# Performance work log

Measured on AMD Instinct MI355X. Metric: run time of the kernel, lower is better.

## Reference

```python
import jax, jax.numpy as jnp
import numpy as np


def setup_inputs() -> dict:
    key = jax.random.key(0)
    k1, k2, k3, k4, k5 = jax.random.split(key, 5)
    S, B, He, Hd, A = 2048, 32, 1024, 1024, 512
    dec_out = jax.random.normal(k1, (B, Hd), dtype=jnp.float32)
    enc_outs = jax.random.normal(k2, (S, B, He), dtype=jnp.float32)
    # parameter scales matching nn.Linear default init (~U(-1/sqrt(fan_in), ...))
    W_enc = jax.random.normal(k3, (A, He), dtype=jnp.float32) / np.sqrt(He)
    W_dec = jax.random.normal(k4, (A, Hd), dtype=jnp.float32) / np.sqrt(Hd)
    att_v = jax.random.normal(k5, (A,), dtype=jnp.float32) / np.sqrt(A)
    return {"dec_out": dec_out, "enc_outs": enc_outs, "W_enc": W_enc,
            "W_dec": W_dec, "att_v": att_v}


def reference(dec_out, enc_outs, W_enc, W_dec, att_v):
    # enc_att: (S, B, A) = enc_outs @ W_enc^T
    enc_att = jnp.einsum('sbh,ah->sba', enc_outs, W_enc)
    # dec_att: (B, A) = dec_out @ W_dec^T, tiled over seq_len
    dec_att = jnp.einsum('bh,ah->ba', dec_out, W_dec)
    # additive score: tanh(enc_att + dec_att) . att_v  -> (B, S)
    dec_enc_att = jnp.tanh(enc_att + dec_att[None, :, :])      # (S, B, A)
    scores = jnp.einsum('sba,a->bs', dec_enc_att, att_v)       # (B, S)
    weights = jax.nn.softmax(scores, axis=-1)                  # (B, S)
    # context: weighted sum of encoder outputs -> (B, He)
    context = jnp.einsum('bs,sbh->bh', weights, enc_outs)
    return context, weights
```

## Files before the change

### kernel.cpp

```cpp
#include <hip/hip_runtime.h>
#include <hip/hip_bf16.h>


typedef float f32x4 __attribute__((ext_vector_type(4)));
typedef __bf16 bf16x8 __attribute__((ext_vector_type(8)));

#define WS_DEC_OFF    0u
#define WS_WIMG_OFF   65536u
#define WS_SCORES_OFF (65536u + 1048576u)
#define WS_PART_OFF   (65536u + 1048576u + 262144u)

#define WAITVM10()  asm volatile("s_waitcnt vmcnt(10)" ::: "memory")
#define WAITVM0()   asm volatile("s_waitcnt vmcnt(0)" ::: "memory")
#define WAITLGKM0() asm volatile("s_waitcnt lgkmcnt(0)" ::: "memory")
#define SBAR()      asm volatile("s_barrier" ::: "memory")

__device__ __forceinline__ void gload_lds16(const void* g, void* l) {
  __builtin_amdgcn_global_load_lds(
      (const __attribute__((address_space(1))) void*)g,
      (__attribute__((address_space(3))) void*)l, 16, 0, 0);
}

__global__ void dec_att_kernel(const float* __restrict__ dec_out,
                               const float* __restrict__ W_dec,
                               float* __restrict__ out) {
  int gtid = blockIdx.x * blockDim.x + threadIdx.x;
  int w = gtid >> 6;
  int lane = gtid & 63;
  int b = w >> 9;
  int a = w & 511;
  const float4* dp = (const float4*)(dec_out + b * 1024);
  const float4* wp = (const float4*)(W_dec + a * 1024);
  float sum = 0.f;
#pragma unroll
  for (int i = 0; i < 4; ++i) {
    float4 x = dp[lane + i * 64];
    float4 y = wp[lane + i * 64];
    sum += x.x * y.x + x.y * y.y + x.z * y.z + x.w * y.w;
  }
#pragma unroll
  for (int m = 32; m; m >>= 1) sum += __shfl_xor(sum, m, 64);
  if (lane == 0) out[b * 512 + a] = sum;
}

__global__ void convert_wenc(const float* __restrict__ W, __bf16* __restrict__ out) {
  int idx = blockIdx.x * 256 + threadIdx.x;
  int kc = idx >> 14;
  int row = (idx >> 5) & 511;
  int j = idx & 31;
  out[idx] = (__bf16)W[row * 1024 + kc * 32 + j];
}

__global__ __launch_bounds__(256, 2) void scores_gemm(
    const float* __restrict__ enc,
    const __bf16* __restrict__ wimg,
    const float* __restrict__ dec_att,
    const float* __restrict__ attv,
    float* __restrict__ scores) {
  __shared__ __align__(16) char smem[73728];
  float (*part)[4] = (float(*)[4])smem;

  const int tid = threadIdx.x;
  const int lane = tid & 63;
  const int wc = tid >> 6;
  const int q = lane >> 4;
  const int c0 = lane & 15;
  const int bm = blockIdx.x;

  f32x4 acc[4][8];
#pragma unroll
  for (int i = 0; i < 4; ++i)
#pragma unroll
    for (int j = 0; j < 8; ++j) acc[i][j] = (f32x4){0.f, 0.f, 0.f, 0.f};

  const int srow = tid >> 2;
  const int sq = tid & 3;
  const float* asrc = enc + (size_t)(bm * 64 + srow) * 1024 + sq * 8;
  const char* bimg = (const char*)wimg;

  int a_roff[4], b_roff[8];
#pragma unroll
  for (int mf = 0; mf < 4; ++mf) a_roff[mf] = (mf * 16 + c0) * 64 + q * 16;
#pragma unroll
  for (int nf = 0; nf < 8; ++nf) b_roff[nf] = (wc * 128 + nf * 16 + c0) * 64 + q * 16;

  {
    const float4* as4 = (const float4*)asrc;
    float4 x = as4[0], y = as4[1];
#pragma unroll
    for (int p = 0; p < 8; ++p)
      gload_lds16(bimg + p * 4096 + tid * 16, smem + 8192 + p * 4096 + tid * 16);
    bf16x8 v;
    v[0] = (__bf16)x.x; v[1] = (__bf16)x.y; v[2] = (__bf16)x.z; v[3] = (__bf16)x.w;
    v[4] = (__bf16)y.x; v[5] = (__bf16)y.y; v[6] = (__bf16)y.z; v[7] = (__bf16)y.w;
    *(bf16x8*)(smem + tid * 16) = v;
    WAITLGKM0();
  }

  for (int t = 0; t < 32; ++t) {
    const int cur = t & 1;
    char* ab = smem + cur * 4096;
    char* bb = smem + 8192 + cur * 32768;
    float4 an0, an1;
    if (t < 31) {
      const float4* as4 = (const float4*)(asrc + (t + 1) * 32);
      an0 = as4[0]; an1 = as4[1];
      const char* bs = bimg + (size_t)(t + 1) * 32768;
      char* bd = smem + 8192 + (cur ^ 1) * 32768;
#pragma unroll
      for (int p = 0; p < 8; ++p)
        gload_lds16(bs + p * 4096 + tid * 16, bd + p * 4096 + tid * 16);
      WAITVM10();
    } else {
      WAITVM0();
    }
    SBAR();
    bf16x8 af[4], bfr[8];
#pragma unroll
    for (int mf = 0; mf < 4; ++mf) af[mf] = *(const bf16x8*)(ab + a_roff[mf]);
#pragma unroll
    for (int nf = 0; nf < 8; ++nf) bfr[nf] = *(const bf16x8*)(bb + b_roff[nf]);
    __builtin_amdgcn_s_setprio(1);
#pragma unroll
    for (int mf = 0; mf < 4; ++mf)
#pragma unroll
      for (int nf = 0; nf < 8; ++nf)
        acc[mf][nf] = __builtin_amdgcn_mfma_f32_16x16x32_bf16(af[mf], bfr[nf],
                                                              acc[mf][nf], 0, 0, 0);
    __builtin_amdgcn_s_setprio(0);
    if (t < 31) {
      bf16x8 v;
      v[0] = (__bf16)an0.x; v[1] = (__bf16)an0.y; v[2] = (__bf16)an0.z; v[3] = (__bf16)an0.w;
      v[4] = (__bf16)an1.x; v[5] = (__bf16)an1.y; v[6] = (__bf16)an1.z; v[7] = (__bf16)an1.w;
      *(bf16x8*)(smem + (cur ^ 1) * 4096 + tid * 16) = v;
    }
    WAITLGKM0();
    SBAR();
  }

  float av[8];
#pragma unroll
  for (int nf = 0; nf < 8; ++nf) av[nf] = attv[wc * 128 + nf * 16 + c0];

#pragma unroll
  for (int mf = 0; mf < 4; ++mf) {
#pragma unroll
    for (int rg = 0; rg < 4; ++rg) {
      const int rl = mf * 16 + q * 4 + rg;
      const int b = rl & 31;
      const float* drow = dec_att + b * 512 + wc * 128 + c0;
      float sum = 0.f;
#pragma unroll
      for (int nf = 0; nf < 8; ++nf) {
        float x = acc[mf][nf][rg] + drow[nf * 16];
        float e = __expf(2.f * x);
        float t = 1.f - 2.f / (e + 1.f);
        sum += t * av[nf];
      }
      sum += __shfl_xor(sum, 1, 64);
      sum += __shfl_xor(sum, 2, 64);
      sum += __shfl_xor(sum, 4, 64);
      sum += __shfl_xor(sum, 8, 64);
      if (c0 == 0) part[rl][wc] = sum;
    }
  }
  __syncthreads();
  if (tid < 64) {
    float tot = part[tid][0] + part[tid][1] + part[tid][2] + part[tid][3];
    int r = bm * 64 + tid;
    scores[(r & 31) * 2048 + (r >> 5)] = tot;
  }
}

__global__ void softmax_kernel(const float* __restrict__ scores,
                               float* __restrict__ weights) {
  const int b = blockIdx.x;
  const int t = threadIdx.x;
  const float4* row = (const float4*)(scores + b * 2048);
  float4 v0 = row[t];
  float4 v1 = row[t + 256];
  float m = fmaxf(fmaxf(fmaxf(v0.x, v0.y), fmaxf(v0.z, v0.w)),
                  fmaxf(fmaxf(v1.x, v1.y), fmaxf(v1.z, v1.w)));
#pragma unroll
  for (int s = 32; s; s >>= 1) m = fmaxf(m, __shfl_xor(m, s, 64));
  __shared__ float redm[4], reds[4];
  if ((t & 63) == 0) redm[t >> 6] = m;
  __syncthreads();
  m = fmaxf(fmaxf(redm[0], redm[1]), fmaxf(redm[2], redm[3]));
  float4 e0, e1;
  e0.x = __expf(v0.x - m); e0.y = __expf(v0.y - m);
  e0.z = __expf(v0.z - m); e0.w = __expf(v0.w - m);
  e1.x = __expf(v1.x - m); e1.y = __expf(v1.y - m);
  e1.z = __expf(v1.z - m); e1.w = __expf(v1.w - m);
  float s8 = e0.x + e0.y + e0.z + e0.w + e1.x + e1.y + e1.z + e1.w;
#pragma unroll
  for (int s = 32; s; s >>= 1) s8 += __shfl_xor(s8, s, 64);
  if ((t & 63) == 0) reds[t >> 6] = s8;
  __syncthreads();
  float inv = 1.f / (reds[0] + reds[1] + reds[2] + reds[3]);
  e0.x *= inv; e0.y *= inv; e0.z *= inv; e0.w *= inv;
  e1.x *= inv; e1.y *= inv; e1.z *= inv; e1.w *= inv;
  float4* wrow = (float4*)(weights + b * 2048);
  wrow[t] = e0;
  wrow[t + 256] = e1;
}

__global__ void ctx_partial(const float* __restrict__ enc,
                            const float* __restrict__ weights,
                            float* __restrict__ part) {
  const int b = blockIdx.x & 31;
  const int sc = blockIdx.x >> 5;
  const int t = threadIdx.x;
  const float* wrow = weights + b * 2048 + sc * 128;
  const char* ebase = (const char*)(enc + ((size_t)(sc * 128) * 32 + b) * 1024) + t * 16;
  float4 acc = {0.f, 0.f, 0.f, 0.f};
#pragma unroll 4
  for (int i = 0; i < 128; ++i) {
    float4 e = *(const float4*)(ebase + (size_t)i * 131072);
    float ws = wrow[i];
    acc.x += ws * e.x; acc.y += ws * e.y; acc.z += ws * e.z; acc.w += ws * e.w;
  }
  *(float4*)(part + (size_t)(sc * 32 + b) * 1024 + t * 4) = acc;
}

__global__ void ctx_reduce(const float* __restrict__ part, float* __restrict__ ctx) {
  int idx = blockIdx.x * 256 + threadIdx.x;
  float s = 0.f;
#pragma unroll
  for (int c = 0; c < 16; ++c) s += part[c * 32768 + idx];
  ctx[idx] = s;
}

extern "C" void kernel_launch(void* const* d_in, const int* in_sizes, int n_in,
                              void* d_out, int out_size, void* d_ws, size_t ws_size,
                              hipStream_t stream) {
  const float* dec_out  = (const float*)d_in[0];
  const float* enc_outs = (const float*)d_in[1];
  const float* W_enc    = (const float*)d_in[2];
  const float* W_dec    = (const float*)d_in[3];
  const float* att_v    = (const float*)d_in[4];

  float* out = (float*)d_out;
  float* ctx = out;
  float* weights = out + 32768;

  char* ws = (char*)d_ws;
  float*  ws_dec    = (float*)(ws + WS_DEC_OFF);
  __bf16* ws_wimg   = (__bf16*)(ws + WS_WIMG_OFF);
  float*  ws_scores = (float*)(ws + WS_SCORES_OFF);
  float*  ws_part   = (float*)(ws + WS_PART_OFF);

  dec_att_kernel<<<4096, 256, 0, stream>>>(dec_out, W_dec, ws_dec);
  convert_wenc<<<2048, 256, 0, stream>>>(W_enc, ws_wimg);
  scores_gemm<<<1024, 256, 0, stream>>>(enc_outs, ws_wimg, ws_dec, att_v, ws_scores);
  softmax_kernel<<<32, 256, 0, stream>>>(ws_scores, weights);
  ctx_partial<<<512, 256, 0, stream>>>(enc_outs, weights, ws_part);
  ctx_reduce<<<128, 256, 0, stream>>>(ws_part, ctx);
}
```

Measured before the change: 184.2 us.

## Load W_enc fragments directly into registers and swizzle A tile in LDS

Stops staging the bf16 W_enc image through LDS with global_load_lds. Each wave now loads its B fragments straight from global memory into registers, double-buffered as current and next sets, and LDS shrinks from 72KB to 8KB. The A tile write and read offsets get an XOR-style swizzle to avoid bank conflicts. This removes LDS traffic for B and the large shared footprint, which may allow more resident blocks, but it adds register pressure from the 16 extra bf16x8 registers. Global loads for B are no longer shared across the four waves and must be fully hidden behind one iteration of MFMA work.

```diff
diff --git a/kernel.cpp b/kernel.cpp
--- a/kernel.cpp
+++ b/kernel.cpp
@@ -10,16 +10,8 @@
 #define WS_SCORES_OFF (65536u + 1048576u)
 #define WS_PART_OFF   (65536u + 1048576u + 262144u)
 
-#define WAITVM10()  asm volatile("s_waitcnt vmcnt(10)" ::: "memory")
-#define WAITVM0()   asm volatile("s_waitcnt vmcnt(0)" ::: "memory")
 #define WAITLGKM0() asm volatile("s_waitcnt lgkmcnt(0)" ::: "memory")
 #define SBAR()      asm volatile("s_barrier" ::: "memory")
-
-__device__ __forceinline__ void gload_lds16(const void* g, void* l) {
-  __builtin_amdgcn_global_load_lds(
-      (const __attribute__((address_space(1))) void*)g,
-      (__attribute__((address_space(3))) void*)l, 16, 0, 0);
-}
 
 __global__ void dec_att_kernel(const float* __restrict__ dec_out,
                                const float* __restrict__ W_dec,
@@ -57,7 +49,7 @@
     const float* __restrict__ dec_att,
     const float* __restrict__ attv,
     float* __restrict__ scores) {
-  __shared__ __align__(16) char smem[73728];
+  __shared__ __align__(16) char smem[8192];
   float (*part)[4] = (float(*)[4])smem;
 
   const int tid = threadIdx.x;
@@ -76,63 +68,61 @@
   const int srow = tid >> 2;
   const int sq = tid & 3;
   const float* asrc = enc + (size_t)(bm * 64 + srow) * 1024 + sq * 8;
-  const char* bimg = (const char*)wimg;
-
-  int a_roff[4], b_roff[8];
-#pragma unroll
-  for (int mf = 0; mf < 4; ++mf) a_roff[mf] = (mf * 16 + c0) * 64 + q * 16;
-#pragma unroll
-  for (int nf = 0; nf < 8; ++nf) b_roff[nf] = (wc * 128 + nf * 16 + c0) * 64 + q * 16;
+  const int a_woff = srow * 64 + (((sq + (srow >> 1)) & 3) << 4);
+  int a_roff[4];
+#pragma unroll
+  for (int mf = 0; mf < 4; ++mf) {
+    const int row = mf * 16 + c0;
+    a_roff[mf] = row * 64 + (((q + (row >> 1)) & 3) << 4);
+  }
+
+  const char* bptr = (const char*)wimg + (wc * 128 + c0) * 64 + q * 16;
+
+  bf16x8 bcur[8], bnxt[8];
 
   {
     const float4* as4 = (const float4*)asrc;
     float4 x = as4[0], y = as4[1];
 #pragma unroll
-    for (int p = 0; p < 8; ++p)
-      gload_lds16(bimg + p * 4096 + tid * 16, smem + 8192 + p * 4096 + tid * 16);
+    for (int nf = 0; nf < 8; ++nf)
+      bcur[nf] = *(const bf16x8*)(bptr + nf * 1024);
     bf16x8 v;
     v[0] = (__bf16)x.x; v[1] = (__bf16)x.y; v[2] = (__bf16)x.z; v[3] = (__bf16)x.w;
     v[4] = (__bf16)y.x; v[5] = (__bf16)y.y; v[6] = (__bf16)y.z; v[7] = (__bf16)y.w;
-    *(bf16x8*)(smem + tid * 16) = v;
-    WAITLGKM0();
-  }
+    *(bf16x8*)(smem + a_woff) = v;
+  }
+  __syncthreads();
 
   for (int t = 0; t < 32; ++t) {
     const int cur = t & 1;
     char* ab = smem + cur * 4096;
-    char* bb = smem + 8192 + cur * 32768;
     float4 an0, an1;
     if (t < 31) {
       const float4* as4 = (const float4*)(asrc + (t + 1) * 32);
       an0 = as4[0]; an1 = as4[1];
-      const char* bs = bimg + (size_t)(t + 1) * 32768;
-      char* bd = smem + 8192 + (cur ^ 1) * 32768;
-#pragma unroll
-      for (int p = 0; p < 8; ++p)
-        gload_lds16(bs + p * 4096 + tid * 16, bd + p * 4096 + tid * 16);
-      WAITVM10();
-    } else {
-      WAITVM0();
+      const char* bs = bptr + (size_t)(t + 1) * 32768;
+#pragma unroll
+      for (int nf = 0; nf < 8; ++nf)
+        bnxt[nf] = *(const bf16x8*)(bs + nf * 1024);
     }
-    SBAR();
-    bf16x8 af[4], bfr[8];
+    bf16x8 af[4];
 #pragma unroll
     for (int mf = 0; mf < 4; ++mf) af[mf] = *(const bf16x8*)(ab + a_roff[mf]);
-#pragma unroll
-    for (int nf = 0; nf < 8; ++nf) bfr[nf] = *(const bf16x8*)(bb + b_roff[nf]);
     __builtin_amdgcn_s_setprio(1);
 #pragma unroll
     for (int mf = 0; mf < 4; ++mf)
 #pragma unroll
       for (int nf = 0; nf < 8; ++nf)
-        acc[mf][nf] = __builtin_amdgcn_mfma_f32_16x16x32_bf16(af[mf], bfr[nf],
+        acc[mf][nf] = __builtin_amdgcn_mfma_f32_16x16x32_bf16(af[mf], bcur[nf],
                                                               acc[mf][nf], 0, 0, 0);
     __builtin_amdgcn_s_setprio(0);
     if (t < 31) {
       bf16x8 v;
       v[0] = (__bf16)an0.x; v[1] = (__bf16)an0.y; v[2] = (__bf16)an0.z; v[3] = (__bf16)an0.w;
       v[4] = (__bf16)an1.x; v[5] = (__bf16)an1.y; v[6] = (__bf16)an1.z; v[7] = (__bf16)an1.w;
-      *(bf16x8*)(smem + (cur ^ 1) * 4096 + tid * 16) = v;
+      *(bf16x8*)(smem + (cur ^ 1) * 4096 + a_woff) = v;
+#pragma unroll
+      for (int nf = 0; nf < 8; ++nf) bcur[nf] = bnxt[nf];
     }
     WAITLGKM0();
     SBAR();
```

Result: faster. 161.8 us (-12.2%).
